# Performance work log

Hardware: AMD Instinct MI355X
Metric: run time of the kernel (lower is better)

The kernel has to match this reference:

```python
import jax, jax.numpy as jnp
import numpy as np

B, C, T, H, W = 8, 128, 16, 32, 32
M, N, CS = 64, 64, 64


def setup_inputs() -> dict:
    key = jax.random.key(0)
    ks = jax.random.split(key, 12)
    s = 0.02
    return {
        "input": jax.random.normal(ks[0], (B, C, T, H, W), dtype=jnp.float32),
        "condition": jax.random.normal(ks[1], (B, CS), dtype=jnp.float32),
        # 1x1x1 Conv3d weights collapse to (out, in) matrices
        "W_phi": jax.random.normal(ks[2], (M, C), dtype=jnp.float32) * s,
        "b_phi": jax.random.normal(ks[3], (M,), dtype=jnp.float32) * s,
        "W_theta": jax.random.normal(ks[4], (N, C), dtype=jnp.float32) * s,
        "b_theta": jax.random.normal(ks[5], (N,), dtype=jnp.float32) * s,
        "W_rho": jax.random.normal(ks[6], (N, C), dtype=jnp.float32) * s,
        "b_rho": jax.random.normal(ks[7], (N,), dtype=jnp.float32) * s,
        "W1": jax.random.normal(ks[8], (CS, CS), dtype=jnp.float32) * s,
        "b1": jax.random.normal(ks[9], (CS,), dtype=jnp.float32) * s,
        "W2": jax.random.normal(ks[10], (H * W, CS), dtype=jnp.float32) * s,
        "b2": jax.random.normal(ks[11], (H * W,), dtype=jnp.float32) * s,
    }


def _pointwise_conv3d(x, Wt, b):
    # Conv3d with kernel=1, stride=1 == channel mixing
    return jnp.einsum('bcthw,oc->bothw', x, Wt) + b[None, :, None, None, None]


def reference(input, condition, W_phi, b_phi, W_theta, b_theta, W_rho, b_rho, W1, b1, W2, b2):
    x = input.reshape(-1, C, T, H, W)
    cond = condition.reshape(x.shape[0], -1)
    A = _pointwise_conv3d(x, W_phi, b_phi)                       # (b,m,t,h,w)
    B0 = _pointwise_conv3d(x, W_theta, b_theta)                  # (b,n,t,h,w)
    Bm = jax.nn.softmax(B0.reshape(B0.shape[0], B0.shape[1], -1), axis=-1).reshape(B0.shape)
    # FC_Cond: Linear+ReLU, Linear+ReLU, then softmax over h*w
    h1 = jax.nn.relu(cond @ W1.T + b1)
    h2 = jax.nn.relu(h1 @ W2.T + b2)
    Cm = jax.nn.softmax(h2, axis=-1).reshape(-1, H, W)           # (b,h,w)
    BC = Bm * Cm[:, None, None, :, :]                            # (b,n,t,h,w)
    AB_T = jnp.einsum('bmthw,bnthw->bmn', A, BC)                 # (b,m,n)
    V = jax.nn.softmax(_pointwise_conv3d(x, W_rho, b_rho), axis=1)
    Z = jnp.einsum('bmn,bnthw->bmthw', AB_T, V)
    attn = jnp.transpose(Bm * V, (0, 1, 3, 4, 2))                # (b,n,h,w,t)
    return (Z, attn)
```

## Files before the change

kernel.cpp:

```cpp
#include <hip/hip_runtime.h>

#define CC 128
#define SB 16384

typedef _Float16 half2_t __attribute__((ext_vector_type(2)));
typedef _Float16 half4_t __attribute__((ext_vector_type(4)));
typedef _Float16 half8_t __attribute__((ext_vector_type(8)));
typedef float    f32x4  __attribute__((ext_vector_type(4)));

#define WH_OFF   0u
#define BIAS_OFF 49152u
#define CM_OFF   50176u
#define SUME_OFF 82944u
#define AB_OFF   86016u
#define PT_OFF   262144u
#define VT_OFF   33816576u

__global__ void k0_setup(const float* __restrict__ cond,
                         const float* __restrict__ W_phi, const float* __restrict__ b_phi,
                         const float* __restrict__ W_theta, const float* __restrict__ b_theta,
                         const float* __restrict__ W_rho, const float* __restrict__ b_rho,
                         const float* __restrict__ W1, const float* __restrict__ b1,
                         const float* __restrict__ W2, const float* __restrict__ b2,
                         char* __restrict__ wsc) {
  __shared__ float sc[64], sh1[64], red[256];
  int t = threadIdx.x, bid = blockIdx.x;
  if (bid < 8) {
    int b = bid;
    if (t < 64) sc[t] = cond[b*64 + t];
    __syncthreads();
    if (t < 64) {
      float acc = b1[t];
      for (int k = 0; k < 64; ++k) acc += sc[k] * W1[t*64 + k];
      sh1[t] = fmaxf(acc, 0.f);
    }
    __syncthreads();
    float ev[4]; float ps = 0.f;
    #pragma unroll
    for (int q = 0; q < 4; ++q) {
      int o = q*256 + t;
      float acc = b2[o];
      for (int k = 0; k < 64; ++k) acc += sh1[k] * W2[o*64 + k];
      ev[q] = __expf(fmaxf(acc, 0.f));
      ps += ev[q];
    }
    red[t] = ps; __syncthreads();
    for (int s = 128; s > 0; s >>= 1) { if (t < s) red[t] += red[t+s]; __syncthreads(); }
    float inv = 1.f / red[0];
    float* cm = (float*)(wsc + CM_OFF);
    #pragma unroll
    for (int q = 0; q < 4; ++q) cm[b*1024 + q*256 + t] = ev[q] * inv;
  } else {
    int r = bid - 8;
    _Float16* wh = (_Float16*)(wsc + WH_OFF);
    for (int i = r*256 + t; i < 24576; i += 2048) {
      int set = i >> 13, mk = i & 8191;
      const float* W = (set == 0) ? W_phi : (set == 1 ? W_theta : W_rho);
      wh[i] = (_Float16)W[mk];
    }
    float* ab = (float*)(wsc + AB_OFF);
    for (int i = r*256 + t; i < 32768; i += 2048) ab[i] = 0.f;
    if (r == 0 && t < 192) {
      float* bias = (float*)(wsc + BIAS_OFF);
      bias[t] = (t < 64) ? b_phi[t] : (t < 128 ? b_theta[t-64] : b_rho[t-128]);
    }
    if (r == 1) {
      float* se = (float*)(wsc + SUME_OFF);
      for (int i = t; i < 512; i += 256) se[i] = 0.f;
    }
  }
}

__global__ __launch_bounds__(256, 2) void kC_main(
    const float* __restrict__ x, const _Float16* __restrict__ wh,
    const float* __restrict__ bias, const float* __restrict__ cm,
    float* __restrict__ sumE, _Float16* __restrict__ vt,
    char* __restrict__ ptb,
    float* __restrict__ abf) {
  __shared__ char smem[35328];
  __shared__ float se_l[256];
  _Float16* Xh  = (_Float16*)smem;
  _Float16* A_l = (_Float16*)smem;
  _Float16* E_l = (_Float16*)(smem + 17408);

  int t = threadIdx.x;
  int lane = t & 63, wv = t >> 6, ln = lane & 15, q = lane >> 4;
  int bid = blockIdx.x, b = bid >> 7, chunk = bid & 127;
  int s0 = chunk * 128;

  const float* xb = x + (size_t)b*CC*SB + s0;
  #pragma unroll
  for (int r = 0; r < 16; ++r) {
    int fid = r*256 + t;
    int c = fid >> 5, s4 = (fid & 31) << 2;
    float4 v = *(const float4*)(xb + (size_t)c*SB + s4);
    half2_t p0 = { (_Float16)v.x, (_Float16)v.y };
    half2_t p1 = { (_Float16)v.z, (_Float16)v.w };
    *(half2_t*)&Xh[c*138 + s4]     = p0;
    *(half2_t*)&Xh[c*138 + s4 + 2] = p1;
  }
  __syncthreads();

  int myp = wv * 32;
  half8_t bf[2][4];
  #pragma unroll
  for (int nt = 0; nt < 2; ++nt) {
    int s = myp + nt*16 + ln;
    #pragma unroll
    for (int kk = 0; kk < 4; ++kk) {
      half8_t h;
      #pragma unroll
      for (int j = 0; j < 8; ++j) h[j] = Xh[(kk*32 + q*8 + j)*138 + s];
      bf[nt][kk] = h;
    }
  }

  int gsl[2] = { s0 + myp + ln, s0 + myp + 16 + ln };
  float cmv[2] = { cm[b*1024 + (gsl[0] & 1023)], cm[b*1024 + (gsl[1] & 1023)] };
  __syncthreads();

  half8_t af[4][4];
  f32x4 d[4][2];
  float ev[4][2][4];

  auto conv = [&](int setoff) {
    #pragma unroll
    for (int mt = 0; mt < 4; ++mt)
      #pragma unroll
      for (int kk = 0; kk < 4; ++kk)
        af[mt][kk] = *(const half8_t*)(wh + setoff + (mt*16 + ln)*128 + kk*32 + q*8);
    #pragma unroll
    for (int mt = 0; mt < 4; ++mt)
      #pragma unroll
      for (int nt = 0; nt < 2; ++nt)
        d[mt][nt] = (f32x4){0.f, 0.f, 0.f, 0.f};
    #pragma unroll
    for (int kk = 0; kk < 4; ++kk)
      #pragma unroll
      for (int mt = 0; mt < 4; ++mt)
        #pragma unroll
        for (int nt = 0; nt < 2; ++nt)
          d[mt][nt] = __builtin_amdgcn_mfma_f32_16x16x32_f16(af[mt][kk], bf[nt][kk],
                                                             d[mt][nt], 0, 0, 0);
  };

  conv(0);
  #pragma unroll
  for (int mt = 0; mt < 4; ++mt) {
    float bv[4]; *(float4*)bv = *(const float4*)(bias + mt*16 + q*4);
    #pragma unroll
    for (int nt = 0; nt < 2; ++nt)
      #pragma unroll
      for (int r = 0; r < 4; ++r)
        A_l[(mt*16 + q*4 + r)*136 + myp + nt*16 + ln] = (_Float16)(d[mt][nt][r] + bv[r]);
  }

  conv(8192);
  float sp[4][4];
  #pragma unroll
  for (int mt = 0; mt < 4; ++mt) {
    float bv[4]; *(float4*)bv = *(const float4*)(bias + 64 + mt*16 + q*4);
    #pragma unroll
    for (int r = 0; r < 4; ++r) {
      #pragma unroll
      for (int nt = 0; nt < 2; ++nt) {
        float e = __expf(d[mt][nt][r] + bv[r]);
        ev[mt][nt][r] = e;
        E_l[(mt*16 + q*4 + r)*136 + myp + nt*16 + ln] = (_Float16)(e * cmv[nt]);
      }
      sp[mt][r] = ev[mt][0][r] + ev[mt][1][r];
    }
  }
  #pragma unroll
  for (int mt = 0; mt < 4; ++mt)
    #pragma unroll
    for (int r = 0; r < 4; ++r) {
      float v = sp[mt][r];
      v += __shfl_xor(v, 1); v += __shfl_xor(v, 2);
      v += __shfl_xor(v, 4); v += __shfl_xor(v, 8);
      sp[mt][r] = v;
    }
  if (ln == 0) {
    #pragma unroll
    for (int mt = 0; mt < 4; ++mt)
      #pragma unroll
      for (int r = 0; r < 4; ++r)
        se_l[wv*64 + mt*16 + q*4 + r] = sp[mt][r];
  }

  conv(16384);
  #pragma unroll
  for (int mt = 0; mt < 4; ++mt) {
    float bv[4]; *(float4*)bv = *(const float4*)(bias + 128 + mt*16 + q*4);
    #pragma unroll
    for (int nt = 0; nt < 2; ++nt)
      #pragma unroll
      for (int r = 0; r < 4; ++r)
        d[mt][nt][r] = __expf(d[mt][nt][r] + bv[r]);
  }
  float cs[2] = {0.f, 0.f};
  #pragma unroll
  for (int mt = 0; mt < 4; ++mt)
    #pragma unroll
    for (int nt = 0; nt < 2; ++nt)
      #pragma unroll
      for (int r = 0; r < 4; ++r) cs[nt] += d[mt][nt][r];
  #pragma unroll
  for (int nt = 0; nt < 2; ++nt) {
    cs[nt] += __shfl_xor(cs[nt], 16);
    cs[nt] += __shfl_xor(cs[nt], 32);
    cs[nt] = 1.f / cs[nt];
  }
  #pragma unroll
  for (int nt = 0; nt < 2; ++nt) {
    size_t grow = (size_t)b*SB + gsl[nt];
    _Float16* vrow = vt + grow*64;
    char* prow = ptb + grow*128;
    #pragma unroll
    for (int mt = 0; mt < 4; ++mt) {
      half4_t hv, hp;
      #pragma unroll
      for (int r = 0; r < 4; ++r) {
        float vv = d[mt][nt][r] * cs[nt];
        hv[r] = (_Float16)vv;
        hp[r] = (_Float16)(vv * ev[mt][nt][r]);
      }
      *(half4_t*)(vrow + mt*16 + q*4) = hv;
      *(half4_t*)(prow + (size_t)(mt*16 + q*4)*2) = hp;
    }
  }
  __syncthreads();

  if (t < 64) {
    float ssum = se_l[t] + se_l[64+t] + se_l[128+t] + se_l[192+t];
    atomicAdd(&sumE[b*64 + t], ssum);
  }

  f32x4 dab[4];
  #pragma unroll
  for (int n2 = 0; n2 < 4; ++n2) dab[n2] = (f32x4){0.f, 0.f, 0.f, 0.f};
  #pragma unroll
  for (int kk = 0; kk < 4; ++kk) {
    half8_t aab = *(half8_t*)&A_l[(wv*16 + ln)*136 + kk*32 + q*8];
    #pragma unroll
    for (int n2 = 0; n2 < 4; ++n2) {
      half8_t bab = *(half8_t*)&E_l[(n2*16 + ln)*136 + kk*32 + q*8];
      dab[n2] = __builtin_amdgcn_mfma_f32_16x16x32_f16(aab, bab, dab[n2], 0, 0, 0);
    }
  }
  float* ab = abf + b*4096;
  #pragma unroll
  for (int n2 = 0; n2 < 4; ++n2)
    #pragma unroll
    for (int r = 0; r < 4; ++r)
      atomicAdd(&ab[(wv*16 + q*4 + r)*64 + n2*16 + ln], dab[n2][r]);
}

__global__ __launch_bounds__(256) void k34(const float* __restrict__ abf,
                                           const _Float16* __restrict__ vt,
                                           const char* __restrict__ ptb,
                                           const float* __restrict__ sumE,
                                           float* __restrict__ out) {
  __shared__ _Float16 sm[256*72];
  int t = threadIdx.x;
  if (blockIdx.x < 512) {
    _Float16* Ah = sm;
    int lane = t & 63, wv = t >> 6, ln = lane & 15, q = lane >> 4;
    int bid = blockIdx.x, b = bid >> 6, chunk = bid & 63;
    int s0 = chunk * 256;
    const float* ab = abf + b*4096;
    const float* se = sumE + b*64;
    #pragma unroll
    for (int r = 0; r < 16; ++r) {
      int idx = r*256 + t;
      int m = idx >> 6, n = idx & 63;
      Ah[m*72 + n] = (_Float16)(ab[idx] * (1024.f / se[n]));
    }
    __syncthreads();
    half8_t a8[4][2];
    #pragma unroll
    for (int mt = 0; mt < 4; ++mt)
      #pragma unroll
      for (int kk = 0; kk < 2; ++kk)
        a8[mt][kk] = *(half8_t*)&Ah[(mt*16 + ln)*72 + kk*32 + q*8];
    int sw = s0 + wv*64;
    #pragma unroll
    for (int nt = 0; nt < 4; ++nt) {
      int sb = sw + nt*16 + ln;
      const _Float16* vrow = vt + ((size_t)b*SB + sb)*64;
      half8_t b8[2];
      b8[0] = *(const half8_t*)(vrow + q*8);
      b8[1] = *(const half8_t*)(vrow + 32 + q*8);
      f32x4 dz[4];
      #pragma unroll
      for (int mt = 0; mt < 4; ++mt) dz[mt] = (f32x4){0.f, 0.f, 0.f, 0.f};
      #pragma unroll
      for (int kk = 0; kk < 2; ++kk)
        #pragma unroll
        for (int mt = 0; mt < 4; ++mt)
          dz[mt] = __builtin_amdgcn_mfma_f32_16x16x32_f16(a8[mt][kk], b8[kk], dz[mt], 0, 0, 0);
      #pragma unroll
      for (int mt = 0; mt < 4; ++mt)
        #pragma unroll
        for (int r = 0; r < 4; ++r)
          out[((size_t)(b*64 + mt*16 + q*4 + r))*SB + sb] = dz[mt][r] * (1.f/1024.f);
    }
  } else {
    _Float16* P_l = sm;
    int bid = blockIdx.x - 512;
    int b = bid >> 6, hw0 = (bid & 63) * 16;
    int st = t >> 4, h = t & 15;
    int s = st*1024 + hw0 + h;
    const char* prow = ptb + ((size_t)b*SB + s)*128;
    #pragma unroll
    for (int c8 = 0; c8 < 8; ++c8)
      *(half8_t*)&P_l[t*72 + c8*8] = *(const half8_t*)(prow + c8*16);
    __syncthreads();
    int n = t >> 2, oc = t & 3;
    float ri = 1.f / sumE[b*64 + n];
    float* orow = out + 8388608 + (size_t)(b*64 + n)*SB + hw0*16;
    #pragma unroll
    for (int i = 0; i < 16; ++i) {
      int j = oc*64 + i*4;
      int hh = j >> 4, stb = j & 15;
      float w[4];
      #pragma unroll
      for (int r = 0; r < 4; ++r)
        w[r] = (float)P_l[((stb + r)*16 + hh)*72 + n] * ri;
      *(float4*)(orow + j) = *(float4*)w;
    }
  }
}

extern "C" void kernel_launch(void* const* d_in, const int* in_sizes, int n_in,
                              void* d_out, int out_size, void* d_ws, size_t ws_size,
                              hipStream_t stream) {
  const float* input   = (const float*)d_in[0];
  const float* cond    = (const float*)d_in[1];
  const float* W_phi   = (const float*)d_in[2];
  const float* b_phi   = (const float*)d_in[3];
  const float* W_theta = (const float*)d_in[4];
  const float* b_theta = (const float*)d_in[5];
  const float* W_rho   = (const float*)d_in[6];
  const float* b_rho   = (const float*)d_in[7];
  const float* W1      = (const float*)d_in[8];
  const float* b1      = (const float*)d_in[9];
  const float* W2      = (const float*)d_in[10];
  const float* b2      = (const float*)d_in[11];
  char* wsc = (char*)d_ws;
  float* out = (float*)d_out;

  const _Float16* wh = (const _Float16*)(wsc + WH_OFF);
  const float* bias = (const float*)(wsc + BIAS_OFF);
  const float* cmp  = (const float*)(wsc + CM_OFF);
  float* sumE  = (float*)(wsc + SUME_OFF);
  float* abf   = (float*)(wsc + AB_OFF);
  _Float16* vt = (_Float16*)(wsc + VT_OFF);

  hipLaunchKernelGGL(k0_setup, dim3(16), dim3(256), 0, stream,
                     cond, W_phi, b_phi, W_theta, b_theta, W_rho, b_rho,
                     W1, b1, W2, b2, wsc);
  hipLaunchKernelGGL(kC_main, dim3(1024), dim3(256), 0, stream,
                     input, wh, bias, cmp, sumE, vt, (char*)(wsc + PT_OFF), abf);
  hipLaunchKernelGGL(k34, dim3(1024), dim3(256), 0, stream,
                     abf, vt, (const char*)(wsc + PT_OFF), sumE, out);
}
```

Before: 204.2 us.

## Load x tile via direct global-to-LDS loads and interleave k34 block roles

The main kernel now stages the fp32 input tile straight into shared memory with global_load_lds, skipping the register round-trip and fp16 conversion on store. The conversion moves to the LDS read that builds MFMA operands. Shared memory grows to 64KB per block, which may cut occupancy below the two blocks per CU requested in launch bounds. Separately, k34 interleaves the Z-GEMM and attention-transpose block types by even/odd block index instead of splitting them into halves, so both kinds of work run at the same time.

```diff
diff --git a/kernel.cpp b/kernel.cpp
--- a/kernel.cpp
+++ b/kernel.cpp
@@ -77,11 +77,11 @@
     float* __restrict__ sumE, _Float16* __restrict__ vt,
     char* __restrict__ ptb,
     float* __restrict__ abf) {
-  __shared__ char smem[35328];
-  __shared__ float se_l[256];
-  _Float16* Xh  = (_Float16*)smem;
+  __shared__ char smem[65536];
+  float*    Xs  = (float*)smem;
   _Float16* A_l = (_Float16*)smem;
   _Float16* E_l = (_Float16*)(smem + 17408);
+  float*    se_l= (float*)(smem + 34816);
 
   int t = threadIdx.x;
   int lane = t & 63, wv = t >> 6, ln = lane & 15, q = lane >> 4;
@@ -89,15 +89,17 @@
   int s0 = chunk * 128;
 
   const float* xb = x + (size_t)b*CC*SB + s0;
-  #pragma unroll
-  for (int r = 0; r < 16; ++r) {
-    int fid = r*256 + t;
-    int c = fid >> 5, s4 = (fid & 31) << 2;
-    float4 v = *(const float4*)(xb + (size_t)c*SB + s4);
-    half2_t p0 = { (_Float16)v.x, (_Float16)v.y };
-    half2_t p1 = { (_Float16)v.z, (_Float16)v.w };
-    *(half2_t*)&Xh[c*138 + s4]     = p0;
-    *(half2_t*)&Xh[c*138 + s4 + 2] = p1;
+  {
+    int l5 = lane >> 5, l31 = lane & 31;
+    #pragma unroll
+    for (int r = 0; r < 16; ++r) {
+      int c0 = r*8 + wv*2;
+      __builtin_amdgcn_global_load_lds(
+          (const __attribute__((address_space(1))) void*)
+              (xb + (size_t)(c0 + l5)*SB + (l31 << 2)),
+          (__attribute__((address_space(3))) void*)(&Xs[c0*128]),
+          16, 0, 0);
+    }
   }
   __syncthreads();
 
@@ -110,7 +112,7 @@
     for (int kk = 0; kk < 4; ++kk) {
       half8_t h;
       #pragma unroll
-      for (int j = 0; j < 8; ++j) h[j] = Xh[(kk*32 + q*8 + j)*138 + s];
+      for (int j = 0; j < 8; ++j) h[j] = (_Float16)Xs[(kk*32 + q*8 + j)*128 + s];
       bf[nt][kk] = h;
     }
   }
@@ -263,10 +265,11 @@
                                            float* __restrict__ out) {
   __shared__ _Float16 sm[256*72];
   int t = threadIdx.x;
-  if (blockIdx.x < 512) {
+  int hid = blockIdx.x >> 1;
+  if ((blockIdx.x & 1) == 0) {
     _Float16* Ah = sm;
     int lane = t & 63, wv = t >> 6, ln = lane & 15, q = lane >> 4;
-    int bid = blockIdx.x, b = bid >> 6, chunk = bid & 63;
+    int b = hid >> 6, chunk = hid & 63;
     int s0 = chunk * 256;
     const float* ab = abf + b*4096;
     const float* se = sumE + b*64;
@@ -307,8 +310,7 @@
     }
   } else {
     _Float16* P_l = sm;
-    int bid = blockIdx.x - 512;
-    int b = bid >> 6, hw0 = (bid & 63) * 16;
+    int b = hid >> 6, hw0 = (hid & 63) * 16;
     int st = t >> 4, h = t & 15;
     int s = st*1024 + hw0 + h;
     const char* prow = ptb + ((size_t)b*SB + s)*128;
```

Result: slower. 208.6 us (+2.1%).
